# Kernel tuning notes

Hardware: AMD Instinct MI355X
Metric: run time of the kernel (lower is better)

The kernel has to match this reference:

```python
import jax, jax.numpy as jnp
import numpy as np

N_NODES = 100000
N_EDGES = 1600000
IN_DIM, HID_DIM, OUT_DIM = 128, 128, 64


def setup_inputs() -> dict:
    key = jax.random.key(0)
    ks = jax.random.split(key, 5)
    x = jax.random.normal(ks[0], (N_NODES, IN_DIM), dtype=jnp.float32)
    edge_index = jax.random.randint(ks[1], (2, N_EDGES), 0, N_NODES, dtype=jnp.int64)
    W1 = jax.random.normal(ks[2], (IN_DIM, HID_DIM), dtype=jnp.float32) * (1.0 / np.sqrt(IN_DIM))
    b1 = jnp.zeros((HID_DIM,), dtype=jnp.float32)
    W2 = jax.random.normal(ks[3], (HID_DIM, OUT_DIM), dtype=jnp.float32) * (1.0 / np.sqrt(HID_DIM))
    b2 = jnp.zeros((OUT_DIM,), dtype=jnp.float32)
    return {"x": x, "edge_index": edge_index, "W1": W1, "b1": b1, "W2": W2, "b2": b2}


def _gcn_conv(h, row, col, norm, b, n_nodes):
    # h: [N, F] already linearly transformed; message = norm_e * h[src]; scatter-add to dst
    msg = h[row] * norm[:, None]                      # [E+N, F]
    out = jax.ops.segment_sum(msg, col, num_segments=n_nodes)
    return out + b


def reference(x, edge_index, W1, b1, W2, b2):
    n = x.shape[0]
    loops = jnp.arange(n, dtype=edge_index.dtype)
    row = jnp.concatenate([edge_index[0], loops])     # sources (incl. self loops)
    col = jnp.concatenate([edge_index[1], loops])     # targets
    # symmetric normalization: deg over targets with unit edge weights
    deg = jax.ops.segment_sum(jnp.ones_like(col, dtype=x.dtype), col, num_segments=n)
    dinv = jnp.where(deg > 0, jax.lax.rsqrt(jnp.maximum(deg, 1.0)), 0.0)
    norm = dinv[row] * dinv[col]                      # [E+N]
    h = jax.nn.relu(_gcn_conv(x @ W1, row, col, norm, b1, n))
    out = _gcn_conv(h @ W2, row, col, norm, b2, n)
    return out.mean(axis=0)                           # [OUT_DIM]
```

## Files before the change

### kernel.cpp

```cpp
#include <hip/hip_runtime.h>

#define N_NODES 100000
#define N_EDGES 1600000
#define IN_DIM 128
#define HID_DIM 128
#define OUT_DIM 64
#define BKT_SHIFT 7
#define BKT_SIZE 128
#define NBKT ((N_NODES + BKT_SIZE - 1) / BKT_SIZE)
#define B1 256
#define HIST_N (NBKT * B1)
#define HIST_N2 (2 * HIST_N)
#define GEMM_BLKS ((N_NODES + 127) / 128)
#define AGG_BLKS 2048
#define NPW 13

typedef float v2f __attribute__((ext_vector_type(2)));
typedef float v4f __attribute__((ext_vector_type(4)));
typedef short v8s __attribute__((ext_vector_type(8)));

__device__ __forceinline__ int permb(int b) { return ((b & 7) << 5) | (b >> 3); }

__device__ __forceinline__ unsigned int f2bf(float f) {
  unsigned int u = __float_as_uint(f);
  return (u + 0x7FFFu + ((u >> 16) & 1u)) >> 16;
}

template <bool HI>
__device__ __forceinline__ v2f cvt8(unsigned int u) {
  return __builtin_amdgcn_cvt_pk_f32_fp8((int)u, HI);
}

__device__ __forceinline__ float wdec(unsigned int p) {
  return __uint_as_float((p >> 17) << 16);
}

__device__ __forceinline__ float redq(float v) {
  v += __shfl_xor(v, 16);
  v += __shfl_xor(v, 32);
  return v;
}

__device__ __forceinline__ void load4(const void* ei, int is64, int half, int base,
                                      int* v) {
  if (is64) {
    const long long* e = (const long long*)ei + (size_t)half * N_EDGES + base;
    longlong2 a = *(const longlong2*)e;
    longlong2 b = *(const longlong2*)(e + 2);
    v[0] = (int)a.x; v[1] = (int)a.y; v[2] = (int)b.x; v[3] = (int)b.y;
  } else {
    const int* e = (const int*)ei + (size_t)half * N_EDGES + base;
    int4 a = *(const int4*)e;
    v[0] = a.x; v[1] = a.y; v[2] = a.z; v[3] = a.w;
  }
}

__device__ __forceinline__ int detect64_block(const unsigned int* ei, int* sh) {
  if (threadIdx.x == 0) *sh = 0;
  __syncthreads();
  if (ei[1 + 2 * threadIdx.x] != 0u) *sh = 1;
  __syncthreads();
  return (*sh == 0) ? 1 : 0;
}

__global__ __launch_bounds__(256) void front_kernel(const float* __restrict__ x,
                                                    const float* __restrict__ W,
                                                    const void* ei,
                                                    unsigned int* __restrict__ G,
                                                    int* hist, float* S) {
  __shared__ __align__(16) char smem[2 * 128 * 136 * 2];
  if (blockIdx.x >= GEMM_BLKS) {
    int* hd = (int*)smem;
    int* hs = hd + NBKT;
    int* sh = hs + NBKT;
    const int hb = blockIdx.x - GEMM_BLKS;
    const int pj = permb(hb);
    if (hb == 0 && threadIdx.x < HID_DIM) S[threadIdx.x] = 0.f;
    const int is64 = detect64_block((const unsigned int*)ei, sh);
    for (int k = threadIdx.x; k < NBKT; k += 256) { hd[k] = 0; hs[k] = 0; }
    __syncthreads();
    for (int g = hb * 256 + threadIdx.x; g < N_EDGES / 4; g += B1 * 256) {
      int r[4], c[4];
      load4(ei, is64, 0, g * 4, r);
      load4(ei, is64, 1, g * 4, c);
#pragma unroll
      for (int k = 0; k < 4; k++) {
        atomicAdd(&hd[c[k] >> BKT_SHIFT], 1);
        atomicAdd(&hs[r[k] >> BKT_SHIFT], 1);
      }
    }
    __syncthreads();
    for (int k = threadIdx.x; k < NBKT; k += 256) {
      hist[k * B1 + pj] = hd[k];
      hist[HIST_N + k * B1 + pj] = hs[k];
    }
    return;
  }
  typedef unsigned short us_row[136];
  us_row* lx = (us_row*)smem;
  us_row* lwt = (us_row*)(smem + 128 * 136 * 2);
  const int t = threadIdx.x;
  const int row0 = blockIdx.x * 128;

  {
    const float4* W4 = (const float4*)W;
    for (int it = 0; it < 16; ++it) {
      int idx = t + 256 * it;
      int k = idx >> 5, c4 = (idx & 31) * 4;
      float4 w = W4[idx];
      lwt[c4 + 0][k] = (unsigned short)f2bf(w.x);
      lwt[c4 + 1][k] = (unsigned short)f2bf(w.y);
      lwt[c4 + 2][k] = (unsigned short)f2bf(w.z);
      lwt[c4 + 3][k] = (unsigned short)f2bf(w.w);
    }
  }
  {
    const float4* x4 = (const float4*)(x + (size_t)row0 * IN_DIM);
    for (int it = 0; it < 16; ++it) {
      int idx = t + 256 * it;
      int r = idx >> 5, kq = (idx & 31) * 4;
      float4 v = make_float4(0.f, 0.f, 0.f, 0.f);
      if (row0 + r < N_NODES) v = x4[idx];
      unsigned int p0 = (f2bf(v.y) << 16) | f2bf(v.x);
      unsigned int p1 = (f2bf(v.w) << 16) | f2bf(v.z);
      *(uint2*)&lx[r][kq] = make_uint2(p0, p1);
    }
  }
  __syncthreads();

  const int lane = t & 63;
  const int wv = t >> 6;
  const int m0 = wv * 32;
  const int lrow = lane & 15;
  const int lk = (lane >> 4) * 8;

  v4f acc[2][8];
#pragma unroll
  for (int si = 0; si < 2; si++)
#pragma unroll
    for (int n = 0; n < 8; n++) acc[si][n] = (v4f){0.f, 0.f, 0.f, 0.f};

#pragma unroll
  for (int kk = 0; kk < 128; kk += 32) {
    v8s a0 = *(const v8s*)&lx[m0 + lrow][kk + lk];
    v8s a1 = *(const v8s*)&lx[m0 + 16 + lrow][kk + lk];
#pragma unroll
    for (int n = 0; n < 8; n++) {
      v8s b = *(const v8s*)&lwt[n * 16 + lrow][kk + lk];
      acc[0][n] = __builtin_amdgcn_mfma_f32_16x16x32_bf16(a0, b, acc[0][n], 0, 0, 0);
      acc[1][n] = __builtin_amdgcn_mfma_f32_16x16x32_bf16(a1, b, acc[1][n], 0, 0, 0);
    }
  }

  unsigned char* G8 = (unsigned char*)G;
#pragma unroll
  for (int si = 0; si < 2; si++)
#pragma unroll
    for (int n = 0; n < 8; n++) {
      int colg = n * 16 + (lane & 15);
#pragma unroll
      for (int i = 0; i < 4; i++) {
        int r = row0 + m0 + si * 16 + (lane >> 4) * 4 + i;
        if (r < N_NODES) {
          float v = acc[si][n][i];
          int pk = __builtin_amdgcn_cvt_pk_fp8_f32(v, v, 0, false);
          G8[(size_t)r * HID_DIM + colg] = (unsigned char)(pk & 0xFF);
        }
      }
    }
}

__global__ void scan1_kernel(int* arr, int* bsum, int n) {
  __shared__ int tmp[256];
  int i = blockIdx.x * 256 + threadIdx.x;
  int v = (i < n) ? arr[i] : 0;
  tmp[threadIdx.x] = v;
  __syncthreads();
  for (int off = 1; off < 256; off <<= 1) {
    int t2 = (threadIdx.x >= off) ? tmp[threadIdx.x - off] : 0;
    __syncthreads();
    tmp[threadIdx.x] += t2;
    __syncthreads();
  }
  if (i < n) arr[i] = tmp[threadIdx.x] - v;
  if (threadIdx.x == 255) bsum[blockIdx.x] = tmp[255];
}

__global__ void scan2_kernel(int* bsum, int nb) {
  __shared__ int tmp[1024];
  const int t = threadIdx.x;
  int v0 = (2 * t < nb) ? bsum[2 * t] : 0;
  int v1 = (2 * t + 1 < nb) ? bsum[2 * t + 1] : 0;
  int s = v0 + v1;
  tmp[t] = s;
  __syncthreads();
  for (int off = 1; off < 1024; off <<= 1) {
    int t2 = (t >= off) ? tmp[t - off] : 0;
    __syncthreads();
    tmp[t] += t2;
    __syncthreads();
  }
  int excl = tmp[t] - s;
  if (2 * t < nb) bsum[2 * t] = excl;
  if (2 * t + 1 < nb) bsum[2 * t + 1] = excl + v0;
}

__global__ __launch_bounds__(256) void scatter_kernel(const void* ei, const int* hist,
                                                      const int* bsum,
                                                      unsigned int* pairs) {
  __shared__ int cd[NBKT], cs[NBKT], sh[1];
  const int is64 = detect64_block((const unsigned int*)ei, sh);
  const int pj = permb(blockIdx.x);
  for (int k = threadIdx.x; k < NBKT; k += 256) {
    cd[k] = hist[k * B1 + pj] + bsum[k];
    cs[k] = hist[HIST_N + k * B1 + pj] + bsum[NBKT + k];
  }
  __syncthreads();
  for (int g = blockIdx.x * 256 + threadIdx.x; g < N_EDGES / 4; g += B1 * 256) {
    int r[4], c[4];
    load4(ei, is64, 0, g * 4, r);
    load4(ei, is64, 1, g * 4, c);
#pragma unroll
    for (int k = 0; k < 4; k++) {
      int pd = atomicAdd(&cd[c[k] >> BKT_SHIFT], 1);
      pairs[pd] = ((unsigned int)(c[k] & (BKT_SIZE - 1)) << 17) | (unsigned int)r[k];
      int ps = atomicAdd(&cs[r[k] >> BKT_SHIFT], 1);
      pairs[ps] = ((unsigned int)(r[k] & (BKT_SIZE - 1)) << 17) | (unsigned int)c[k];
    }
  }
}

__global__ __launch_bounds__(256) void csrA_kernel(const int* hist, const int* bsum,
                                                   const unsigned int* pairs,
                                                   int* rowptr, float* dinv) {
  __shared__ int cnt[BKT_SIZE], sc[BKT_SIZE];
  const int k = blockIdx.x;
  const int base = hist[k * B1] + bsum[k];
  const int end = (k == NBKT - 1) ? N_EDGES : hist[(k + 1) * B1] + bsum[k + 1];
  const int nseg = end - base;
  const int l = threadIdx.x;
  if (l < BKT_SIZE) cnt[l] = 0;
  __syncthreads();
  for (int i = l; i < nseg; i += 256) atomicAdd(&cnt[pairs[base + i] >> 17], 1);
  __syncthreads();
  if (l < BKT_SIZE) sc[l] = cnt[l];
  __syncthreads();
  for (int off = 1; off < BKT_SIZE; off <<= 1) {
    int v = (l < BKT_SIZE && l >= off) ? sc[l - off] : 0;
    __syncthreads();
    if (l < BKT_SIZE) sc[l] += v;
    __syncthreads();
  }
  if (l < BKT_SIZE) {
    int excl = sc[l] - cnt[l];
    int v = k * BKT_SIZE + l;
    if (v < N_NODES) {
      rowptr[v] = base + excl;
      dinv[v] = rsqrtf((float)(cnt[l] + 1));
    }
  }
  if (k == NBKT - 1 && l == 0) rowptr[N_NODES] = N_EDGES;
}

__global__ __launch_bounds__(256) void csrBout_kernel(const int* hist, const int* bsum,
                                                      const unsigned int* pairs,
                                                      const int* __restrict__ rowptr,
                                                      const float* __restrict__ dinv,
                                                      unsigned int* __restrict__ csr,
                                                      float* __restrict__ wacc) {
  if (blockIdx.x < NBKT) {
    __shared__ int cur[BKT_SIZE];
    const int k = blockIdx.x;
    const int base = hist[k * B1] + bsum[k];
    const int end = (k == NBKT - 1) ? N_EDGES : hist[(k + 1) * B1] + bsum[k + 1];
    const int nseg = end - base;
    const int l = threadIdx.x;
    if (l < BKT_SIZE) {
      int v = k * BKT_SIZE + l;
      cur[l] = (v < N_NODES) ? rowptr[v] : 0;
    }
    __syncthreads();
    for (int i = l; i < nseg; i += 256) {
      unsigned int pk = pairs[base + i];
      unsigned int src = pk & 0x1FFFFu;
      int pos = atomicAdd(&cur[pk >> 17], 1);
      unsigned int bits = f2bf(dinv[src]);
      csr[pos] = (bits << 17) | src;
    }
    return;
  }
  __shared__ float fb[BKT_SIZE];
  const int k = blockIdx.x - NBKT;
  const int base = hist[HIST_N + k * B1] + bsum[NBKT + k];
  const int end =
      (k == NBKT - 1) ? 2 * N_EDGES : hist[HIST_N + (k + 1) * B1] + bsum[NBKT + k + 1];
  if (threadIdx.x < BKT_SIZE) fb[threadIdx.x] = 0.f;
  __syncthreads();
  for (int i = base + threadIdx.x; i < end; i += 256) {
    unsigned int pk = pairs[i];
    atomicAdd(&fb[pk >> 17], dinv[pk & 0x1FFFFu]);
  }
  __syncthreads();
  int v = k * BKT_SIZE + threadIdx.x;
  if (threadIdx.x < BKT_SIZE && v < N_NODES) wacc[v] = fb[threadIdx.x];
}

__global__ __launch_bounds__(256) void aggregate_kernel(
    const unsigned int* __restrict__ G, const int* __restrict__ rowptr,
    const unsigned int* __restrict__ csr, const float* __restrict__ dinv,
    const float* __restrict__ wacc, const float* __restrict__ b1,
    float* __restrict__ S) {
  const int lane = threadIdx.x & 63;
  const int q = lane >> 4;
  const int r = lane & 15;
  const int wid = blockIdx.x * 4 + (threadIdx.x >> 6);
  const int c0 = wid * NPW;
  const uint2* __restrict__ G2 = (const uint2*)G;

  int rp = 0;
  float dvv = 0.f, wvv = 0.f;
  {
    const int ci = c0 + lane;
    if (lane <= NPW && ci <= N_NODES) rp = rowptr[ci];
    if (lane < NPW && ci < N_NODES) { dvv = dinv[ci]; wvv = wacc[ci]; }
  }
  const float4 bA = ((const float4*)b1)[2 * r];
  const float4 bB = ((const float4*)b1)[2 * r + 1];

  v2f s01 = {0.f, 0.f}, s23 = {0.f, 0.f}, s45 = {0.f, 0.f}, s67 = {0.f, 0.f};

  const int nn = (c0 < N_NODES) ? min(NPW, N_NODES - c0) : 0;

  int sNxt = __shfl(rp, 0);
  int eNxt = __shfl(rp, 1);
  unsigned int pwNxt = 0;
  if (nn > 0 && sNxt + lane < eNxt)
    pwNxt = __builtin_nontemporal_load(&csr[sNxt + lane]);

  for (int k = 0; k < nn; ++k) {
    const int sc = sNxt;
    const int cnum = eNxt - sNxt;
    unsigned int pw = pwNxt;
    const float d = __shfl(dvv, k);
    const float wa = __shfl(wvv, k);
    if (k + 1 < nn) {
      sNxt = __shfl(rp, k + 1);
      eNxt = __shfl(rp, k + 2);
      pwNxt = 0;
      if (sNxt + lane < eNxt)
        pwNxt = __builtin_nontemporal_load(&csr[sNxt + lane]);
    }

    v2f a01 = {0.f, 0.f}, a23 = {0.f, 0.f}, a45 = {0.f, 0.f}, a67 = {0.f, 0.f};
    if (q == 0) {
      uint2 g = G2[(size_t)(c0 + k) * 16 + r];
      a01 += cvt8<false>(g.x) * d; a23 += cvt8<true>(g.x) * d;
      a45 += cvt8<false>(g.y) * d; a67 += cvt8<true>(g.y) * d;
    }

    for (int j0 = 0; j0 < cnum; j0 += 64) {
      if (j0 > 0) {
        pw = 0;
        if (j0 + lane < cnum)
          pw = __builtin_nontemporal_load(&csr[sc + j0 + lane]);
      }
      const int m = min(64, cnum - j0);
      int i = 0;
      for (; i + 16 <= m; i += 16) {
        float w[4];
        uint2 g[4];
#pragma unroll
        for (int t = 0; t < 4; ++t) {
          unsigned int p = __shfl(pw, i + 4 * t + q);
          w[t] = wdec(p);
          g[t] = G2[(size_t)(p & 0x1FFFFu) * 16 + r];
        }
#pragma unroll
        for (int t = 0; t < 4; ++t) {
          a01 += cvt8<false>(g[t].x) * w[t]; a23 += cvt8<true>(g[t].x) * w[t];
          a45 += cvt8<false>(g[t].y) * w[t]; a67 += cvt8<true>(g[t].y) * w[t];
        }
      }
      if (i < m) {
        float w[4];
        uint2 g[4];
#pragma unroll
        for (int t = 0; t < 4; ++t) {
          const int e = i + 4 * t + q;
          unsigned int p = __shfl(pw, e & 63);
          const bool vld = e < m;
          w[t] = vld ? wdec(p) : 0.f;
          g[t] = make_uint2(0u, 0u);
          if (vld) g[t] = G2[(size_t)(p & 0x1FFFFu) * 16 + r];
        }
#pragma unroll
        for (int t = 0; t < 4; ++t) {
          a01 += cvt8<false>(g[t].x) * w[t]; a23 += cvt8<true>(g[t].x) * w[t];
          a45 += cvt8<false>(g[t].y) * w[t]; a67 += cvt8<true>(g[t].y) * w[t];
        }
      }
    }

    a01.x = redq(a01.x); a01.y = redq(a01.y);
    a23.x = redq(a23.x); a23.y = redq(a23.y);
    a45.x = redq(a45.x); a45.y = redq(a45.y);
    a67.x = redq(a67.x); a67.y = redq(a67.y);

    if (q == 0) {
      const float wc = d * (wa + d);
      s01.x += wc * fmaxf(fmaf(d, a01.x, bA.x), 0.f);
      s01.y += wc * fmaxf(fmaf(d, a01.y, bA.y), 0.f);
      s23.x += wc * fmaxf(fmaf(d, a23.x, bA.z), 0.f);
      s23.y += wc * fmaxf(fmaf(d, a23.y, bA.w), 0.f);
      s45.x += wc * fmaxf(fmaf(d, a45.x, bB.x), 0.f);
      s45.y += wc * fmaxf(fmaf(d, a45.y, bB.y), 0.f);
      s67.x += wc * fmaxf(fmaf(d, a67.x, bB.z), 0.f);
      s67.y += wc * fmaxf(fmaf(d, a67.y, bB.w), 0.f);
    }
  }

  __shared__ float ls[HID_DIM];
  if (threadIdx.x < HID_DIM) ls[threadIdx.x] = 0.f;
  __syncthreads();
  if (q == 0) {
    atomicAdd(&ls[8 * r + 0], s01.x); atomicAdd(&ls[8 * r + 1], s01.y);
    atomicAdd(&ls[8 * r + 2], s23.x); atomicAdd(&ls[8 * r + 3], s23.y);
    atomicAdd(&ls[8 * r + 4], s45.x); atomicAdd(&ls[8 * r + 5], s45.y);
    atomicAdd(&ls[8 * r + 6], s67.x); atomicAdd(&ls[8 * r + 7], s67.y);
  }
  __syncthreads();
  if (threadIdx.x < HID_DIM) atomicAdd(&S[threadIdx.x], ls[threadIdx.x]);
}

__global__ void finish_kernel(const float* __restrict__ S, const float* __restrict__ W2,
                              const float* __restrict__ b2, float* __restrict__ out) {
  int j = threadIdx.x;
  float acc = 0.f;
  for (int k = 0; k < HID_DIM; k++) acc += S[k] * W2[k * OUT_DIM + j];
  out[j] = acc * (1.0f / N_NODES) + b2[j];
}

extern "C" void kernel_launch(void* const* d_in, const int* in_sizes, int n_in,
                              void* d_out, int out_size, void* d_ws, size_t ws_size,
                              hipStream_t stream) {
  const float* x  = (const float*)d_in[0];
  const void*  ei = d_in[1];
  const float* W1 = (const float*)d_in[2];
  const float* b1 = (const float*)d_in[3];
  const float* W2 = (const float*)d_in[4];
  const float* b2 = (const float*)d_in[5];
  float* out = (float*)d_out;

  char* p = (char*)d_ws;
  size_t off = 0;
  auto alloc = [&](size_t bytes) -> void* {
    void* r = p + off;
    off = (off + bytes + 63) & ~(size_t)63;
    return r;
  };
  int*   hist   = (int*)alloc((size_t)HIST_N2 * 4);
  int*   bsum   = (int*)alloc(2048 * 4);
  unsigned int* pairs = (unsigned int*)alloc((size_t)2 * N_EDGES * 4);
  int*   rowptr = (int*)alloc(((size_t)N_NODES + 1) * 4);
  unsigned int* csr = (unsigned int*)alloc((size_t)N_EDGES * 4);
  float* dinv   = (float*)alloc((size_t)N_NODES * 4);
  float* wacc   = (float*)alloc((size_t)N_NODES * 4);
  float* S      = (float*)alloc(HID_DIM * 4);
  unsigned int* G = (unsigned int*)alloc((size_t)N_NODES * HID_DIM);
  (void)ws_size; (void)n_in; (void)in_sizes; (void)out_size;

  const int NBH = HIST_N2 / 256;

  front_kernel<<<GEMM_BLKS + B1, 256, 0, stream>>>(x, W1, ei, G, hist, S);
  scan1_kernel<<<NBH, 256, 0, stream>>>(hist, bsum, HIST_N2);
  scan2_kernel<<<1, 1024, 0, stream>>>(bsum, NBH);
  scatter_kernel<<<B1, 256, 0, stream>>>(ei, hist, bsum, pairs);
  csrA_kernel<<<NBKT, 256, 0, stream>>>(hist, bsum, pairs, rowptr, dinv);
  csrBout_kernel<<<2 * NBKT, 256, 0, stream>>>(hist, bsum, pairs, rowptr, dinv, csr,
                                               wacc);
  aggregate_kernel<<<AGG_BLKS, 256, 0, stream>>>(G, rowptr, csr, dinv, wacc, b1, S);
  finish_kernel<<<1, 64, 0, stream>>>(S, W2, b2, out);
}
```

Baseline: 270.4 us.

## Software-pipeline aggregate gathers across nodes with double-buffered fetch/consume

Restructures the per-wave aggregation loop into a flat stream of 16-edge steps spanning node boundaries. Each step's gathers are issued one step ahead into alternating register buffers (A/B), so memory latency overlaps accumulation, including across node transitions. Edge weights are packed as bf16 pairs and the bias is moved into shared memory. This adds control-flow complexity and register pressure, and nodes with few edges still pay a full 16-edge step.

After: 264.5 us. 2.2% less time.

```diff
diff --git a/kernel.cpp b/kernel.cpp
--- a/kernel.cpp
+++ b/kernel.cpp
@@ -29,10 +29,6 @@
 template <bool HI>
 __device__ __forceinline__ v2f cvt8(unsigned int u) {
   return __builtin_amdgcn_cvt_pk_f32_fp8((int)u, HI);
-}
-
-__device__ __forceinline__ float wdec(unsigned int p) {
-  return __uint_as_float((p >> 17) << 16);
 }
 
 __device__ __forceinline__ float redq(float v) {
@@ -310,6 +306,14 @@
     const unsigned int* __restrict__ csr, const float* __restrict__ dinv,
     const float* __restrict__ wacc, const float* __restrict__ b1,
     float* __restrict__ S) {
+  __shared__ float lb[HID_DIM];
+  __shared__ float ls[HID_DIM];
+  if (threadIdx.x < HID_DIM) {
+    lb[threadIdx.x] = b1[threadIdx.x];
+    ls[threadIdx.x] = 0.f;
+  }
+  __syncthreads();
+
   const int lane = threadIdx.x & 63;
   const int q = lane >> 4;
   const int r = lane & 15;
@@ -324,104 +328,125 @@
     if (lane <= NPW && ci <= N_NODES) rp = rowptr[ci];
     if (lane < NPW && ci < N_NODES) { dvv = dinv[ci]; wvv = wacc[ci]; }
   }
-  const float4 bA = ((const float4*)b1)[2 * r];
-  const float4 bB = ((const float4*)b1)[2 * r + 1];
 
   v2f s01 = {0.f, 0.f}, s23 = {0.f, 0.f}, s45 = {0.f, 0.f}, s67 = {0.f, 0.f};
-
   const int nn = (c0 < N_NODES) ? min(NPW, N_NODES - c0) : 0;
 
-  int sNxt = __shfl(rp, 0);
-  int eNxt = __shfl(rp, 1);
-  unsigned int pwNxt = 0;
-  if (nn > 0 && sNxt + lane < eNxt)
-    pwNxt = __builtin_nontemporal_load(&csr[sNxt + lane]);
-
-  for (int k = 0; k < nn; ++k) {
-    const int sc = sNxt;
-    const int cnum = eNxt - sNxt;
-    unsigned int pw = pwNxt;
-    const float d = __shfl(dvv, k);
-    const float wa = __shfl(wvv, k);
-    if (k + 1 < nn) {
-      sNxt = __shfl(rp, k + 1);
-      eNxt = __shfl(rp, k + 2);
-      pwNxt = 0;
-      if (sNxt + lane < eNxt)
-        pwNxt = __builtin_nontemporal_load(&csr[sNxt + lane]);
-    }
-
+  if (nn > 0) {
+    int kF = 0, jF = 0;
+    const int sF0 = __shfl(rp, 0);
+    int cnumF = __shfl(rp, 1) - sF0;
+    int SF = max(1, (cnumF + 15) >> 4);
+    unsigned int pwW = 0;
+    if (lane < cnumF) pwW = __builtin_nontemporal_load(&csr[sF0 + lane]);
+    int sN = __shfl(rp, 1);
+    int eN = __shfl(rp, 2);
+    unsigned int pwN = 0;
+    if (1 < nn && sN + lane < eN) pwN = __builtin_nontemporal_load(&csr[sN + lane]);
+
+    int kC = 0, jC = 0;
+    int SC = SF;
+    float dC = __shfl(dvv, 0), waC = __shfl(wvv, 0);
     v2f a01 = {0.f, 0.f}, a23 = {0.f, 0.f}, a45 = {0.f, 0.f}, a67 = {0.f, 0.f};
-    if (q == 0) {
-      uint2 g = G2[(size_t)(c0 + k) * 16 + r];
-      a01 += cvt8<false>(g.x) * d; a23 += cvt8<true>(g.x) * d;
-      a45 += cvt8<false>(g.y) * d; a67 += cvt8<true>(g.y) * d;
-    }
-
-    for (int j0 = 0; j0 < cnum; j0 += 64) {
-      if (j0 > 0) {
-        pw = 0;
-        if (j0 + lane < cnum)
-          pw = __builtin_nontemporal_load(&csr[sc + j0 + lane]);
-      }
-      const int m = min(64, cnum - j0);
-      int i = 0;
-      for (; i + 16 <= m; i += 16) {
-        float w[4];
-        uint2 g[4];
-#pragma unroll
-        for (int t = 0; t < 4; ++t) {
-          unsigned int p = __shfl(pw, i + 4 * t + q);
-          w[t] = wdec(p);
-          g[t] = G2[(size_t)(p & 0x1FFFFu) * 16 + r];
+
+    uint2 gA[4], gB[4], gSA, gSB;
+    unsigned int wpA[2], wpB[2];
+
+    auto FETCH = [&](uint2(&g)[4], unsigned int(&wp)[2], uint2& gS) {
+      if (jF != 0 && (jF & 3) == 0) {
+        const int sAbs = __shfl(rp, kF) + (jF << 4);
+        pwW = 0;
+        if ((jF << 4) + lane < cnumF)
+          pwW = __builtin_nontemporal_load(&csr[sAbs + lane]);
+      }
+      const int base = (jF & 3) << 4;
+      const int eg0 = (jF << 4) + q;
+      unsigned int wb[4];
+#pragma unroll
+      for (int t = 0; t < 4; ++t) {
+        const unsigned int p = __shfl(pwW, base + 4 * t + q);
+        const bool vld = eg0 + 4 * t < cnumF;
+        wb[t] = vld ? ((p >> 17) << 16) : 0u;
+        g[t] = make_uint2(0u, 0u);
+        if (vld) g[t] = G2[(size_t)(p & 0x1FFFFu) * 16 + r];
+      }
+      wp[0] = wb[0] | (wb[1] >> 16);
+      wp[1] = wb[2] | (wb[3] >> 16);
+      if (jF == 0) {
+        gS = make_uint2(0u, 0u);
+        if (q == 0) gS = G2[(size_t)(c0 + kF) * 16 + r];
+      }
+      if (jF + 1 < SF) { jF++; return; }
+      kF++; jF = 0;
+      if (kF < nn) {
+        pwW = pwN;
+        cnumF = eN - sN;
+        SF = max(1, (cnumF + 15) >> 4);
+        if (kF + 1 < nn) {
+          sN = __shfl(rp, kF + 1);
+          eN = __shfl(rp, kF + 2);
+          pwN = 0;
+          if (sN + lane < eN) pwN = __builtin_nontemporal_load(&csr[sN + lane]);
         }
-#pragma unroll
-        for (int t = 0; t < 4; ++t) {
-          a01 += cvt8<false>(g[t].x) * w[t]; a23 += cvt8<true>(g[t].x) * w[t];
-          a45 += cvt8<false>(g[t].y) * w[t]; a67 += cvt8<true>(g[t].y) * w[t];
-        }
-      }
-      if (i < m) {
-        float w[4];
-        uint2 g[4];
-#pragma unroll
-        for (int t = 0; t < 4; ++t) {
-          const int e = i + 4 * t + q;
-          unsigned int p = __shfl(pw, e & 63);
-          const bool vld = e < m;
-          w[t] = vld ? wdec(p) : 0.f;
-          g[t] = make_uint2(0u, 0u);
-          if (vld) g[t] = G2[(size_t)(p & 0x1FFFFu) * 16 + r];
-        }
-#pragma unroll
-        for (int t = 0; t < 4; ++t) {
-          a01 += cvt8<false>(g[t].x) * w[t]; a23 += cvt8<true>(g[t].x) * w[t];
-          a45 += cvt8<false>(g[t].y) * w[t]; a67 += cvt8<true>(g[t].y) * w[t];
-        }
-      }
-    }
-
-    a01.x = redq(a01.x); a01.y = redq(a01.y);
-    a23.x = redq(a23.x); a23.y = redq(a23.y);
-    a45.x = redq(a45.x); a45.y = redq(a45.y);
-    a67.x = redq(a67.x); a67.y = redq(a67.y);
-
-    if (q == 0) {
-      const float wc = d * (wa + d);
-      s01.x += wc * fmaxf(fmaf(d, a01.x, bA.x), 0.f);
-      s01.y += wc * fmaxf(fmaf(d, a01.y, bA.y), 0.f);
-      s23.x += wc * fmaxf(fmaf(d, a23.x, bA.z), 0.f);
-      s23.y += wc * fmaxf(fmaf(d, a23.y, bA.w), 0.f);
-      s45.x += wc * fmaxf(fmaf(d, a45.x, bB.x), 0.f);
-      s45.y += wc * fmaxf(fmaf(d, a45.y, bB.y), 0.f);
-      s67.x += wc * fmaxf(fmaf(d, a67.x, bB.z), 0.f);
-      s67.y += wc * fmaxf(fmaf(d, a67.y, bB.w), 0.f);
-    }
-  }
-
-  __shared__ float ls[HID_DIM];
-  if (threadIdx.x < HID_DIM) ls[threadIdx.x] = 0.f;
-  __syncthreads();
+      }
+    };
+
+    auto CONSUME = [&](const uint2(&g)[4], const unsigned int(&wp)[2],
+                       const uint2& gS) -> bool {
+      const float w0 = __uint_as_float(wp[0] & 0xFFFF0000u);
+      const float w1 = __uint_as_float(wp[0] << 16);
+      const float w2 = __uint_as_float(wp[1] & 0xFFFF0000u);
+      const float w3 = __uint_as_float(wp[1] << 16);
+      a01 += cvt8<false>(g[0].x) * w0; a23 += cvt8<true>(g[0].x) * w0;
+      a45 += cvt8<false>(g[0].y) * w0; a67 += cvt8<true>(g[0].y) * w0;
+      a01 += cvt8<false>(g[1].x) * w1; a23 += cvt8<true>(g[1].x) * w1;
+      a45 += cvt8<false>(g[1].y) * w1; a67 += cvt8<true>(g[1].y) * w1;
+      a01 += cvt8<false>(g[2].x) * w2; a23 += cvt8<true>(g[2].x) * w2;
+      a45 += cvt8<false>(g[2].y) * w2; a67 += cvt8<true>(g[2].y) * w2;
+      a01 += cvt8<false>(g[3].x) * w3; a23 += cvt8<true>(g[3].x) * w3;
+      a45 += cvt8<false>(g[3].y) * w3; a67 += cvt8<true>(g[3].y) * w3;
+      if (jC == 0 && q == 0) {
+        a01 += cvt8<false>(gS.x) * dC; a23 += cvt8<true>(gS.x) * dC;
+        a45 += cvt8<false>(gS.y) * dC; a67 += cvt8<true>(gS.y) * dC;
+      }
+      if (jC + 1 < SC) { jC++; return true; }
+      const float A0 = redq(a01.x), A1 = redq(a01.y);
+      const float A2 = redq(a23.x), A3 = redq(a23.y);
+      const float A4 = redq(a45.x), A5 = redq(a45.y);
+      const float A6 = redq(a67.x), A7 = redq(a67.y);
+      if (q == 0) {
+        const float wc = dC * (waC + dC);
+        const float* bb = &lb[8 * r];
+        s01.x += wc * fmaxf(fmaf(dC, A0, bb[0]), 0.f);
+        s01.y += wc * fmaxf(fmaf(dC, A1, bb[1]), 0.f);
+        s23.x += wc * fmaxf(fmaf(dC, A2, bb[2]), 0.f);
+        s23.y += wc * fmaxf(fmaf(dC, A3, bb[3]), 0.f);
+        s45.x += wc * fmaxf(fmaf(dC, A4, bb[4]), 0.f);
+        s45.y += wc * fmaxf(fmaf(dC, A5, bb[5]), 0.f);
+        s67.x += wc * fmaxf(fmaf(dC, A6, bb[6]), 0.f);
+        s67.y += wc * fmaxf(fmaf(dC, A7, bb[7]), 0.f);
+      }
+      a01 = (v2f){0.f, 0.f}; a23 = (v2f){0.f, 0.f};
+      a45 = (v2f){0.f, 0.f}; a67 = (v2f){0.f, 0.f};
+      kC++; jC = 0;
+      if (kC >= nn) return false;
+      const int s_ = __shfl(rp, kC);
+      const int cnumC = __shfl(rp, kC + 1) - s_;
+      SC = max(1, (cnumC + 15) >> 4);
+      dC = __shfl(dvv, kC);
+      waC = __shfl(wvv, kC);
+      return true;
+    };
+
+    FETCH(gA, wpA, gSA);
+    for (;;) {
+      if (kF < nn) FETCH(gB, wpB, gSB);
+      if (!CONSUME(gA, wpA, gSA)) break;
+      if (kF < nn) FETCH(gA, wpA, gSA);
+      if (!CONSUME(gB, wpB, gSB)) break;
+    }
+  }
+
   if (q == 0) {
     atomicAdd(&ls[8 * r + 0], s01.x); atomicAdd(&ls[8 * r + 1], s01.y);
     atomicAdd(&ls[8 * r + 2], s23.x); atomicAdd(&ls[8 * r + 3], s23.y);
```

## Split fp8 feature matrix into column quarters and aggregate one quarter per wave

Applied to the files above, without the earlier changes.

The GEMM epilogue now writes the fp8 hidden features in a column-blocked layout, four slabs of 32 columns each stored node-major. In the aggregation kernel each block handles one column quarter, each lane gathers 4 bytes, and 8 edges are processed in parallel per wave, with more nodes per wave (NPW 13→49). Each gathered slab is small, which is meant to improve cache hit rates for the random neighbor gathers. In exchange the CSR rows are re-read once per quarter, a wider cross-lane reduction is needed, and the load balance across waves changes.

Result: slower. 311.0 us (+15.0%).

```diff
diff --git a/kernel.cpp b/kernel.cpp
--- a/kernel.cpp
+++ b/kernel.cpp
@@ -13,7 +13,7 @@
 #define HIST_N2 (2 * HIST_N)
 #define GEMM_BLKS ((N_NODES + 127) / 128)
 #define AGG_BLKS 2048
-#define NPW 13
+#define NPW 49
 
 typedef float v2f __attribute__((ext_vector_type(2)));
 typedef float v4f __attribute__((ext_vector_type(4)));
@@ -33,12 +33,6 @@
 
 __device__ __forceinline__ float wdec(unsigned int p) {
   return __uint_as_float((p >> 17) << 16);
-}
-
-__device__ __forceinline__ float redq(float v) {
-  v += __shfl_xor(v, 16);
-  v += __shfl_xor(v, 32);
-  return v;
 }
 
 __device__ __forceinline__ void load4(const void* ei, int is64, int half, int base,
@@ -164,7 +158,8 @@
         if (r < N_NODES) {
           float v = acc[si][n][i];
           int pk = __builtin_amdgcn_cvt_pk_fp8_f32(v, v, 0, false);
-          G8[(size_t)r * HID_DIM + colg] = (unsigned char)(pk & 0xFF);
+          G8[((size_t)(colg >> 5) * N_NODES + r) * 32 + (colg & 31)] =
+              (unsigned char)(pk & 0xFF);
         }
       }
     }
@@ -310,12 +305,22 @@
     const unsigned int* __restrict__ csr, const float* __restrict__ dinv,
     const float* __restrict__ wacc, const float* __restrict__ b1,
     float* __restrict__ S) {
+  __shared__ float lb[HID_DIM];
+  __shared__ float ls[HID_DIM];
+  if (threadIdx.x < HID_DIM) {
+    lb[threadIdx.x] = b1[threadIdx.x];
+    ls[threadIdx.x] = 0.f;
+  }
+  __syncthreads();
+
   const int lane = threadIdx.x & 63;
-  const int q = lane >> 4;
-  const int r = lane & 15;
-  const int wid = blockIdx.x * 4 + (threadIdx.x >> 6);
-  const int c0 = wid * NPW;
-  const uint2* __restrict__ G2 = (const uint2*)G;
+  const int cl = lane & 7;
+  const int slot = lane >> 3;
+  const int b = blockIdx.x;
+  const int q = (b & 7) >> 1;
+  const int wq = ((b >> 3) << 3) + ((b & 1) << 2) + (threadIdx.x >> 6);
+  const int c0 = wq * NPW;
+  const unsigned int* __restrict__ Gq = G + (size_t)q * N_NODES * 8;
 
   int rp = 0;
   float dvv = 0.f, wvv = 0.f;
@@ -324,112 +329,109 @@
     if (lane <= NPW && ci <= N_NODES) rp = rowptr[ci];
     if (lane < NPW && ci < N_NODES) { dvv = dinv[ci]; wvv = wacc[ci]; }
   }
-  const float4 bA = ((const float4*)b1)[2 * r];
-  const float4 bB = ((const float4*)b1)[2 * r + 1];
-
-  v2f s01 = {0.f, 0.f}, s23 = {0.f, 0.f}, s45 = {0.f, 0.f}, s67 = {0.f, 0.f};
-
+
+  v2f sLo = {0.f, 0.f}, sHi = {0.f, 0.f};
   const int nn = (c0 < N_NODES) ? min(NPW, N_NODES - c0) : 0;
 
-  int sNxt = __shfl(rp, 0);
-  int eNxt = __shfl(rp, 1);
-  unsigned int pwNxt = 0;
-  if (nn > 0 && sNxt + lane < eNxt)
-    pwNxt = __builtin_nontemporal_load(&csr[sNxt + lane]);
+  int sNxt = __shfl(rp, 0), eNxt = __shfl(rp, 1);
+  unsigned int pwNxt = 0, gSNxt = 0;
+  if (nn > 0) {
+    if (lane < eNxt - sNxt) pwNxt = __builtin_nontemporal_load(&csr[sNxt + lane]);
+    if (slot == 0) gSNxt = Gq[(unsigned)c0 * 8 + cl];
+  }
 
   for (int k = 0; k < nn; ++k) {
-    const int sc = sNxt;
+    const int s0 = sNxt;
     const int cnum = eNxt - sNxt;
     unsigned int pw = pwNxt;
-    const float d = __shfl(dvv, k);
-    const float wa = __shfl(wvv, k);
+    const unsigned int gS = gSNxt;
+    const float d = __shfl(dvv, k), wa = __shfl(wvv, k);
     if (k + 1 < nn) {
       sNxt = __shfl(rp, k + 1);
       eNxt = __shfl(rp, k + 2);
       pwNxt = 0;
-      if (sNxt + lane < eNxt)
-        pwNxt = __builtin_nontemporal_load(&csr[sNxt + lane]);
-    }
-
-    v2f a01 = {0.f, 0.f}, a23 = {0.f, 0.f}, a45 = {0.f, 0.f}, a67 = {0.f, 0.f};
-    if (q == 0) {
-      uint2 g = G2[(size_t)(c0 + k) * 16 + r];
-      a01 += cvt8<false>(g.x) * d; a23 += cvt8<true>(g.x) * d;
-      a45 += cvt8<false>(g.y) * d; a67 += cvt8<true>(g.y) * d;
-    }
-
-    for (int j0 = 0; j0 < cnum; j0 += 64) {
-      if (j0 > 0) {
-        pw = 0;
-        if (j0 + lane < cnum)
-          pw = __builtin_nontemporal_load(&csr[sc + j0 + lane]);
-      }
-      const int m = min(64, cnum - j0);
-      int i = 0;
-      for (; i + 16 <= m; i += 16) {
-        float w[4];
-        uint2 g[4];
+      if (lane < eNxt - sNxt) pwNxt = __builtin_nontemporal_load(&csr[sNxt + lane]);
+      if (slot == 0) gSNxt = Gq[(unsigned)(c0 + k + 1) * 8 + cl];
+    }
+
+    v2f aLo = {0.f, 0.f}, aHi = {0.f, 0.f};
+    if (slot == 0) {
+      aLo = cvt8<false>(gS) * d;
+      aHi = cvt8<true>(gS) * d;
+    }
+
+    int j0 = 0;
+    int wlen = min(64, cnum);
+    for (;;) {
+      {
+        unsigned int gb[4];
+        float wb[4];
 #pragma unroll
         for (int t = 0; t < 4; ++t) {
-          unsigned int p = __shfl(pw, i + 4 * t + q);
-          w[t] = wdec(p);
-          g[t] = G2[(size_t)(p & 0x1FFFFu) * 16 + r];
+          const int e = 8 * t + slot;
+          const unsigned int p = __shfl(pw, e);
+          const bool v = e < wlen;
+          wb[t] = v ? wdec(p) : 0.f;
+          gb[t] = 0u;
+          if (v) gb[t] = Gq[(unsigned)(p & 0x1FFFFu) * 8 + cl];
         }
 #pragma unroll
         for (int t = 0; t < 4; ++t) {
-          a01 += cvt8<false>(g[t].x) * w[t]; a23 += cvt8<true>(g[t].x) * w[t];
-          a45 += cvt8<false>(g[t].y) * w[t]; a67 += cvt8<true>(g[t].y) * w[t];
+          aLo += cvt8<false>(gb[t]) * wb[t];
+          aHi += cvt8<true>(gb[t]) * wb[t];
         }
       }
-      if (i < m) {
-        float w[4];
-        uint2 g[4];
+      if (wlen > 32) {
+        unsigned int gb[4];
+        float wb[4];
 #pragma unroll
         for (int t = 0; t < 4; ++t) {
-          const int e = i + 4 * t + q;
-          unsigned int p = __shfl(pw, e & 63);
-          const bool vld = e < m;
-          w[t] = vld ? wdec(p) : 0.f;
-          g[t] = make_uint2(0u, 0u);
-          if (vld) g[t] = G2[(size_t)(p & 0x1FFFFu) * 16 + r];
+          const int e = 32 + 8 * t + slot;
+          const unsigned int p = __shfl(pw, e);
+          const bool v = e < wlen;
+          wb[t] = v ? wdec(p) : 0.f;
+          gb[t] = 0u;
+          if (v) gb[t] = Gq[(unsigned)(p & 0x1FFFFu) * 8 + cl];
         }
 #pragma unroll
         for (int t = 0; t < 4; ++t) {
-          a01 += cvt8<false>(g[t].x) * w[t]; a23 += cvt8<true>(g[t].x) * w[t];
-          a45 += cvt8<false>(g[t].y) * w[t]; a67 += cvt8<true>(g[t].y) * w[t];
+          aLo += cvt8<false>(gb[t]) * wb[t];
+          aHi += cvt8<true>(gb[t]) * wb[t];
         }
       }
-    }
-
-    a01.x = redq(a01.x); a01.y = redq(a01.y);
-    a23.x = redq(a23.x); a23.y = redq(a23.y);
-    a45.x = redq(a45.x); a45.y = redq(a45.y);
-    a67.x = redq(a67.x); a67.y = redq(a67.y);
-
-    if (q == 0) {
+      j0 += 64;
+      if (j0 >= cnum) break;
+      wlen = min(64, cnum - j0);
+      pw = 0;
+      if (lane < wlen) pw = __builtin_nontemporal_load(&csr[s0 + j0 + lane]);
+    }
+
+#define RED3(v) \
+  v += __shfl_xor(v, 8); v += __shfl_xor(v, 16); v += __shfl_xor(v, 32);
+    RED3(aLo.x) RED3(aLo.y) RED3(aHi.x) RED3(aHi.y)
+#undef RED3
+
+    if (slot == 0) {
       const float wc = d * (wa + d);
-      s01.x += wc * fmaxf(fmaf(d, a01.x, bA.x), 0.f);
-      s01.y += wc * fmaxf(fmaf(d, a01.y, bA.y), 0.f);
-      s23.x += wc * fmaxf(fmaf(d, a23.x, bA.z), 0.f);
-      s23.y += wc * fmaxf(fmaf(d, a23.y, bA.w), 0.f);
-      s45.x += wc * fmaxf(fmaf(d, a45.x, bB.x), 0.f);
-      s45.y += wc * fmaxf(fmaf(d, a45.y, bB.y), 0.f);
-      s67.x += wc * fmaxf(fmaf(d, a67.x, bB.z), 0.f);
-      s67.y += wc * fmaxf(fmaf(d, a67.y, bB.w), 0.f);
-    }
-  }
-
-  __shared__ float ls[HID_DIM];
-  if (threadIdx.x < HID_DIM) ls[threadIdx.x] = 0.f;
-  __syncthreads();
-  if (q == 0) {
-    atomicAdd(&ls[8 * r + 0], s01.x); atomicAdd(&ls[8 * r + 1], s01.y);
-    atomicAdd(&ls[8 * r + 2], s23.x); atomicAdd(&ls[8 * r + 3], s23.y);
-    atomicAdd(&ls[8 * r + 4], s45.x); atomicAdd(&ls[8 * r + 5], s45.y);
-    atomicAdd(&ls[8 * r + 6], s67.x); atomicAdd(&ls[8 * r + 7], s67.y);
-  }
-  __syncthreads();
-  if (threadIdx.x < HID_DIM) atomicAdd(&S[threadIdx.x], ls[threadIdx.x]);
+      const float* bb = &lb[q * 32 + 4 * cl];
+      sLo.x += wc * fmaxf(fmaf(d, aLo.x, bb[0]), 0.f);
+      sLo.y += wc * fmaxf(fmaf(d, aLo.y, bb[1]), 0.f);
+      sHi.x += wc * fmaxf(fmaf(d, aHi.x, bb[2]), 0.f);
+      sHi.y += wc * fmaxf(fmaf(d, aHi.y, bb[3]), 0.f);
+    }
+  }
+
+  if (slot == 0) {
+    atomicAdd(&ls[q * 32 + 4 * cl + 0], sLo.x);
+    atomicAdd(&ls[q * 32 + 4 * cl + 1], sLo.y);
+    atomicAdd(&ls[q * 32 + 4 * cl + 2], sHi.x);
+    atomicAdd(&ls[q * 32 + 4 * cl + 3], sHi.y);
+  }
+  __syncthreads();
+  if (threadIdx.x < 32) {
+    const int col = q * 32 + threadIdx.x;
+    atomicAdd(&S[col], ls[col]);
+  }
 }
 
 __global__ void finish_kernel(const float* __restrict__ S, const float* __restrict__ W2,
```

## Remap aggregation to one edge per wave with double-buffered 8-edge gathers

Applied to the files above, without the earlier changes.

Changes the aggregate kernel's lane mapping. All 64 lanes now gather one neighbor row together, two fp8 features per lane, instead of four edges in parallel with eight features per lane. That removes the per-node cross-quad shuffle reduction and the quad-0 predication. Neighbor gathers run in batches of eight with a ping-pong register buffer so the next batch's loads overlap the current batch's accumulation, and the next node's self row is prefetched. The block-level shared-memory atomics are replaced by a per-wave shared array summed by 128 threads. The cost is about four times as many narrow 2-byte gather instructions per edge, plus wasted zero-weight loads when a degree is not a multiple of eight.

New measurement: 321.0 us. 18.7% more time.

```diff
diff --git a/kernel.cpp b/kernel.cpp
--- a/kernel.cpp
+++ b/kernel.cpp
@@ -29,16 +29,6 @@
 template <bool HI>
 __device__ __forceinline__ v2f cvt8(unsigned int u) {
   return __builtin_amdgcn_cvt_pk_f32_fp8((int)u, HI);
-}
-
-__device__ __forceinline__ float wdec(unsigned int p) {
-  return __uint_as_float((p >> 17) << 16);
-}
-
-__device__ __forceinline__ float redq(float v) {
-  v += __shfl_xor(v, 16);
-  v += __shfl_xor(v, 32);
-  return v;
 }
 
 __device__ __forceinline__ void load4(const void* ei, int is64, int half, int base,
@@ -310,12 +300,12 @@
     const unsigned int* __restrict__ csr, const float* __restrict__ dinv,
     const float* __restrict__ wacc, const float* __restrict__ b1,
     float* __restrict__ S) {
+  __shared__ float lsw[4][HID_DIM];
   const int lane = threadIdx.x & 63;
-  const int q = lane >> 4;
-  const int r = lane & 15;
-  const int wid = blockIdx.x * 4 + (threadIdx.x >> 6);
+  const int wv = threadIdx.x >> 6;
+  const int wid = blockIdx.x * 4 + wv;
   const int c0 = wid * NPW;
-  const uint2* __restrict__ G2 = (const uint2*)G;
+  const unsigned short* __restrict__ Gu = (const unsigned short*)G;
 
   int rp = 0;
   float dvv = 0.f, wvv = 0.f;
@@ -324,112 +314,82 @@
     if (lane <= NPW && ci <= N_NODES) rp = rowptr[ci];
     if (lane < NPW && ci < N_NODES) { dvv = dinv[ci]; wvv = wacc[ci]; }
   }
-  const float4 bA = ((const float4*)b1)[2 * r];
-  const float4 bB = ((const float4*)b1)[2 * r + 1];
-
-  v2f s01 = {0.f, 0.f}, s23 = {0.f, 0.f}, s45 = {0.f, 0.f}, s67 = {0.f, 0.f};
-
+  const v2f bl = *(const v2f*)&b1[2 * lane];
+  v2f s = {0.f, 0.f};
   const int nn = (c0 < N_NODES) ? min(NPW, N_NODES - c0) : 0;
 
-  int sNxt = __shfl(rp, 0);
-  int eNxt = __shfl(rp, 1);
+  int sCur = __shfl(rp, 0);
+  int eCur = __shfl(rp, 1);
   unsigned int pwNxt = 0;
-  if (nn > 0 && sNxt + lane < eNxt)
-    pwNxt = __builtin_nontemporal_load(&csr[sNxt + lane]);
+  unsigned int gsNxt = 0;
+  if (nn > 0) {
+    if (lane < eCur - sCur) pwNxt = __builtin_nontemporal_load(&csr[sCur + lane]);
+    gsNxt = Gu[(unsigned)c0 * 64u + lane];
+  }
 
   for (int k = 0; k < nn; ++k) {
-    const int sc = sNxt;
-    const int cnum = eNxt - sNxt;
+    const int st = sCur;
+    const int deg = eCur - sCur;
     unsigned int pw = pwNxt;
+    const unsigned int gs = gsNxt;
     const float d = __shfl(dvv, k);
     const float wa = __shfl(wvv, k);
     if (k + 1 < nn) {
-      sNxt = __shfl(rp, k + 1);
-      eNxt = __shfl(rp, k + 2);
+      sCur = eCur;
+      eCur = __shfl(rp, k + 2);
       pwNxt = 0;
-      if (sNxt + lane < eNxt)
-        pwNxt = __builtin_nontemporal_load(&csr[sNxt + lane]);
-    }
-
-    v2f a01 = {0.f, 0.f}, a23 = {0.f, 0.f}, a45 = {0.f, 0.f}, a67 = {0.f, 0.f};
-    if (q == 0) {
-      uint2 g = G2[(size_t)(c0 + k) * 16 + r];
-      a01 += cvt8<false>(g.x) * d; a23 += cvt8<true>(g.x) * d;
-      a45 += cvt8<false>(g.y) * d; a67 += cvt8<true>(g.y) * d;
-    }
-
-    for (int j0 = 0; j0 < cnum; j0 += 64) {
-      if (j0 > 0) {
-        pw = 0;
-        if (j0 + lane < cnum)
-          pw = __builtin_nontemporal_load(&csr[sc + j0 + lane]);
+      if (lane < eCur - sCur) pwNxt = __builtin_nontemporal_load(&csr[sCur + lane]);
+      gsNxt = Gu[(unsigned)(c0 + k + 1) * 64u + lane];
+    }
+
+    v2f a = cvt8<false>(gs) * d;
+    int j0 = 0;
+    for (;;) {
+      const int m = min(64, deg - j0);
+      unsigned int gA[8], gB[8];
+      float wA[8], wB[8];
+#define LD8(gv, wv, base)                                       \
+  _Pragma("unroll") for (int t = 0; t < 8; ++t) {               \
+    const unsigned int p = __shfl(pw, (base) + t);              \
+    wv[t] = __uint_as_float((p >> 17) << 16);                   \
+    gv[t] = Gu[(unsigned)(p & 0x1FFFFu) * 64u + lane];          \
+  }
+#define CONS8(gv, wv)                                           \
+  _Pragma("unroll") for (int t = 0; t < 8; ++t) {               \
+    a += cvt8<false>(gv[t]) * wv[t];                            \
+  }
+      LD8(gA, wA, 0)
+      int i = 0;
+      for (;;) {
+        if (i + 8 < m) { LD8(gB, wB, i + 8) }
+        CONS8(gA, wA)
+        i += 8;
+        if (i >= m) break;
+        if (i + 8 < m) { LD8(gA, wA, i + 8) }
+        CONS8(gB, wB)
+        i += 8;
+        if (i >= m) break;
       }
-      const int m = min(64, cnum - j0);
-      int i = 0;
-      for (; i + 16 <= m; i += 16) {
-        float w[4];
-        uint2 g[4];
-#pragma unroll
-        for (int t = 0; t < 4; ++t) {
-          unsigned int p = __shfl(pw, i + 4 * t + q);
-          w[t] = wdec(p);
-          g[t] = G2[(size_t)(p & 0x1FFFFu) * 16 + r];
-        }
-#pragma unroll
-        for (int t = 0; t < 4; ++t) {
-          a01 += cvt8<false>(g[t].x) * w[t]; a23 += cvt8<true>(g[t].x) * w[t];
-          a45 += cvt8<false>(g[t].y) * w[t]; a67 += cvt8<true>(g[t].y) * w[t];
-        }
-      }
-      if (i < m) {
-        float w[4];
-        uint2 g[4];
-#pragma unroll
-        for (int t = 0; t < 4; ++t) {
-          const int e = i + 4 * t + q;
-          unsigned int p = __shfl(pw, e & 63);
-          const bool vld = e < m;
-          w[t] = vld ? wdec(p) : 0.f;
-          g[t] = make_uint2(0u, 0u);
-          if (vld) g[t] = G2[(size_t)(p & 0x1FFFFu) * 16 + r];
-        }
-#pragma unroll
-        for (int t = 0; t < 4; ++t) {
-          a01 += cvt8<false>(g[t].x) * w[t]; a23 += cvt8<true>(g[t].x) * w[t];
-          a45 += cvt8<false>(g[t].y) * w[t]; a67 += cvt8<true>(g[t].y) * w[t];
-        }
-      }
-    }
-
-    a01.x = redq(a01.x); a01.y = redq(a01.y);
-    a23.x = redq(a23.x); a23.y = redq(a23.y);
-    a45.x = redq(a45.x); a45.y = redq(a45.y);
-    a67.x = redq(a67.x); a67.y = redq(a67.y);
-
-    if (q == 0) {
-      const float wc = d * (wa + d);
-      s01.x += wc * fmaxf(fmaf(d, a01.x, bA.x), 0.f);
-      s01.y += wc * fmaxf(fmaf(d, a01.y, bA.y), 0.f);
-      s23.x += wc * fmaxf(fmaf(d, a23.x, bA.z), 0.f);
-      s23.y += wc * fmaxf(fmaf(d, a23.y, bA.w), 0.f);
-      s45.x += wc * fmaxf(fmaf(d, a45.x, bB.x), 0.f);
-      s45.y += wc * fmaxf(fmaf(d, a45.y, bB.y), 0.f);
-      s67.x += wc * fmaxf(fmaf(d, a67.x, bB.z), 0.f);
-      s67.y += wc * fmaxf(fmaf(d, a67.y, bB.w), 0.f);
-    }
-  }
-
-  __shared__ float ls[HID_DIM];
-  if (threadIdx.x < HID_DIM) ls[threadIdx.x] = 0.f;
-  __syncthreads();
-  if (q == 0) {
-    atomicAdd(&ls[8 * r + 0], s01.x); atomicAdd(&ls[8 * r + 1], s01.y);
-    atomicAdd(&ls[8 * r + 2], s23.x); atomicAdd(&ls[8 * r + 3], s23.y);
-    atomicAdd(&ls[8 * r + 4], s45.x); atomicAdd(&ls[8 * r + 5], s45.y);
-    atomicAdd(&ls[8 * r + 6], s67.x); atomicAdd(&ls[8 * r + 7], s67.y);
-  }
-  __syncthreads();
-  if (threadIdx.x < HID_DIM) atomicAdd(&S[threadIdx.x], ls[threadIdx.x]);
+#undef LD8
+#undef CONS8
+      j0 += 64;
+      if (j0 >= deg) break;
+      pw = 0;
+      if (lane < deg - j0) pw = __builtin_nontemporal_load(&csr[st + j0 + lane]);
+    }
+    const float wc = d * (wa + d);
+    s.x += wc * fmaxf(fmaf(d, a.x, bl.x), 0.f);
+    s.y += wc * fmaxf(fmaf(d, a.y, bl.y), 0.f);
+  }
+
+  lsw[wv][2 * lane + 0] = s.x;
+  lsw[wv][2 * lane + 1] = s.y;
+  __syncthreads();
+  if (threadIdx.x < HID_DIM) {
+    const float v = lsw[0][threadIdx.x] + lsw[1][threadIdx.x] +
+                    lsw[2][threadIdx.x] + lsw[3][threadIdx.x];
+    atomicAdd(&S[threadIdx.x], v);
+  }
 }
 
 __global__ void finish_kernel(const float* __restrict__ S, const float* __restrict__ W2,
```
